# Kernel optimization log

Hardware: AMD Instinct MI355X
Metric: run time of the kernel (lower is better)

Reference implementation:

```python
import jax, jax.numpy as jnp
import numpy as np

NUM_HEADS = 4
NUM_GROUPS = 8
EPS = 1e-5


def setup_inputs() -> dict:
    key = jax.random.key(0)
    ks = jax.random.split(key, 5)
    B, C, H, W = 16, 512, 32, 32
    s = 1.0 / np.sqrt(C)
    return {
        "x": jax.random.normal(ks[0], (B, C, H, W), dtype=jnp.float32),
        "norm_w": jnp.ones((C,), jnp.float32),
        "norm_b": jnp.zeros((C,), jnp.float32),
        "q_w": jax.random.normal(ks[1], (C, C), jnp.float32) * s,
        "q_b": jnp.zeros((C,), jnp.float32),
        "k_w": jax.random.normal(ks[2], (C, C), jnp.float32) * s,
        "k_b": jnp.zeros((C,), jnp.float32),
        "v_w": jax.random.normal(ks[3], (C, C), jnp.float32) * s,
        "v_b": jnp.zeros((C,), jnp.float32),
        "p_w": jax.random.normal(ks[4], (C, C), jnp.float32) * s,
        "p_b": jnp.zeros((C,), jnp.float32),
    }


def _group_norm(x, w, b):
    # x: (B, C, N) -> GroupNorm over (C//G, N) per group
    B, C, N = x.shape
    g = x.reshape(B, NUM_GROUPS, C // NUM_GROUPS, N)
    mean = g.mean(axis=(2, 3), keepdims=True)
    var = g.var(axis=(2, 3), keepdims=True)
    g = (g - mean) * jax.lax.rsqrt(var + EPS)
    x = g.reshape(B, C, N)
    return x * w[None, :, None] + b[None, :, None]


def reference(x, norm_w, norm_b, q_w, q_b, k_w, k_b, v_w, v_b, p_w, p_b):
    B, C, H, W = x.shape
    N = H * W
    Ch = C // NUM_HEADS  # channels per head
    h = _group_norm(x.reshape(B, C, N), norm_w, norm_b)
    # 1x1 Conv1d == channel matmul: (o c, b c n -> b o n)
    q = jnp.einsum('oc,bcn->bon', q_w, h) + q_b[None, :, None]
    k = jnp.einsum('oc,bcn->bon', k_w, h) + k_b[None, :, None]
    v = jnp.einsum('oc,bcn->bon', v_w, h) + v_b[None, :, None]
    q = q.reshape(B, NUM_HEADS, Ch, N)
    k = k.reshape(B, NUM_HEADS, Ch, N)
    v = v.reshape(B, NUM_HEADS, Ch, N)
    attn = jnp.einsum('bhcn,bhcm->bhnm', q, k) * (1.0 / np.sqrt(Ch))
    attn = jax.nn.softmax(attn, axis=-1)
    out = jnp.einsum('bhnm,bhcm->bhcn', attn, v).reshape(B, C, N)
    out = jnp.einsum('oc,bcn->bon', p_w, out) + p_b[None, :, None]
    return x + out.reshape(B, C, H, W)
```

## Files before the change

kernel.cpp:

```cpp
#include <hip/hip_runtime.h>
#include <hip/hip_bf16.h>
#include <math.h>

#define B_    16
#define C_    512
#define N_    1024
#define G_    8
#define HEADS 4
#define CH    128
#define EPS   1e-5f

typedef __attribute__((ext_vector_type(8))) short short8;
typedef __attribute__((ext_vector_type(4))) float f32x4;
typedef __attribute__((ext_vector_type(16))) float f32x16;
typedef __attribute__((ext_vector_type(4))) int i32x4;

__device__ __forceinline__ unsigned short f2bf(float f) {
  union { float f; unsigned int i; } x; x.f = f;
  unsigned int r = x.i + 0x7FFFu + ((x.i >> 16) & 1u);
  return (unsigned short)(r >> 16);
}

__global__ __launch_bounds__(256) void gn_stats(const float* __restrict__ x,
                                                float* __restrict__ stats) {
  int bg = blockIdx.x;
  const float4* p4 = (const float4*)(x + (size_t)bg * (C_ / G_) * N_);
  const int n4 = (C_ / G_) * N_ / 4;
  float s = 0.f, ss = 0.f;
  for (int i = threadIdx.x; i < n4; i += 256) {
    float4 v = p4[i];
    s  += v.x + v.y + v.z + v.w;
    ss += v.x * v.x + v.y * v.y + v.z * v.z + v.w * v.w;
  }
  for (int o = 32; o; o >>= 1) { s += __shfl_down(s, o); ss += __shfl_down(ss, o); }
  __shared__ float ls[4], lss[4];
  int wid = threadIdx.x >> 6, lane = threadIdx.x & 63;
  if (lane == 0) { ls[wid] = s; lss[wid] = ss; }
  __syncthreads();
  if (threadIdx.x == 0) {
    float S = ls[0] + ls[1] + ls[2] + ls[3];
    float SS = lss[0] + lss[1] + lss[2] + lss[3];
    const float inv = 1.f / ((C_ / G_) * N_);
    float mean = S * inv;
    float var = SS * inv - mean * mean;
    stats[bg * 2]     = mean;
    stats[bg * 2 + 1] = rsqrtf(var + EPS);
  }
}

__global__ __launch_bounds__(256) void conv_w(const float* __restrict__ q, const float* __restrict__ k,
                                              const float* __restrict__ v, const float* __restrict__ p,
                                              const float* __restrict__ qb, const float* __restrict__ kb,
                                              unsigned short* __restrict__ dst,
                                              float* __restrict__ qkb) {
  const int n = C_ * C_;
  int i = blockIdx.x * 256 + threadIdx.x;
  if (i < n) {
    dst[i]         = f2bf(q[i]);
    dst[n + i]     = f2bf(k[i]);
    dst[2 * n + i] = f2bf(v[i]);
    dst[3 * n + i] = f2bf(p[i]);
  }
  if (i < 1024) qkb[i] = (i < 512) ? qb[i] : kb[i - 512];
}

__global__ __launch_bounds__(256) void gn_apply(const float* __restrict__ x,
                                                const float* __restrict__ stats,
                                                const float* __restrict__ gw,
                                                const float* __restrict__ gb,
                                                unsigned short* __restrict__ hT) {
  __shared__ float T[64][65];
  int b = blockIdx.z, c0 = blockIdx.y * 64, n0 = blockIdx.x * 64;
  int g = c0 / (C_ / G_);
  float mean = stats[(b * G_ + g) * 2], rstd = stats[(b * G_ + g) * 2 + 1];
  int t = threadIdx.x;
  for (int it = 0; it < 4; it++) {
    int L = it * 256 + t;
    int cc = L >> 4, nf = L & 15;
    float4 v = *(const float4*)&x[((size_t)b * C_ + c0 + cc) * N_ + n0 + nf * 4];
    float sw = gw[c0 + cc] * rstd, sb = gb[c0 + cc] - mean * sw;
    T[cc][nf * 4 + 0] = v.x * sw + sb;
    T[cc][nf * 4 + 1] = v.y * sw + sb;
    T[cc][nf * 4 + 2] = v.z * sw + sb;
    T[cc][nf * 4 + 3] = v.w * sw + sb;
  }
  __syncthreads();
  for (int it = 0; it < 4; it++) {
    int L = it * 256 + t;
    int nn = L >> 4, cv = L & 15;
    ushort4 o;
    o.x = f2bf(T[cv * 4 + 0][nn]);
    o.y = f2bf(T[cv * 4 + 1][nn]);
    o.z = f2bf(T[cv * 4 + 2][nn]);
    o.w = f2bf(T[cv * 4 + 3][nn]);
    *(ushort4*)&hT[((size_t)b * N_ + n0 + nn) * C_ + c0 + cv * 4] = o;
  }
}

template <bool OUT_BF16, bool BIAS_I, bool RESID>
__global__ __launch_bounds__(256) void gemm_tn(const unsigned short* __restrict__ A,
                                               const unsigned short* __restrict__ Bt,
                                               const float* __restrict__ bias,
                                               const float* __restrict__ resid,
                                               void* __restrict__ out,
                                               int Ncols, int K,
                                               long aBS, long bBS, long oBS) {
  __shared__ __align__(16) unsigned short As[128 * 64];
  __shared__ __align__(16) unsigned short Bs[128 * 64];
  const int b = blockIdx.z;
  const int i0 = blockIdx.y * 128, j0 = blockIdx.x * 128;
  const unsigned short* Ab = A + (size_t)b * aBS + (size_t)i0 * K;
  const unsigned short* Bb = Bt + (size_t)b * bBS + (size_t)j0 * K;
  const int t = threadIdx.x, w = t >> 6, l = t & 63;
  const int wi = (w >> 1) * 64, wj = (w & 1) * 64;
  const int lr = l & 15, lk = (l >> 4) * 8;
  const int srow = l >> 3, scol = (l & 7) * 8;

  f32x4 acc[4][4];
  const f32x4 zf = {0.f, 0.f, 0.f, 0.f};
#pragma unroll
  for (int m = 0; m < 4; m++)
#pragma unroll
    for (int n = 0; n < 4; n++) acc[m][n] = zf;

  for (int kt = 0; kt < K; kt += 64) {
    __syncthreads();
#pragma unroll
    for (int i = 0; i < 4; i++) {
      int seg = w * 4 + i;
      int row = seg * 8 + srow;
      __builtin_amdgcn_global_load_lds(
          (const __attribute__((address_space(1))) void*)&Ab[(size_t)row * K + kt + scol],
          (__attribute__((address_space(3))) void*)&As[seg * 512], 16, 0, 0);
      __builtin_amdgcn_global_load_lds(
          (const __attribute__((address_space(1))) void*)&Bb[(size_t)row * K + kt + scol],
          (__attribute__((address_space(3))) void*)&Bs[seg * 512], 16, 0, 0);
    }
    __syncthreads();
#pragma unroll
    for (int ks = 0; ks < 64; ks += 32) {
      short8 af[4], bf[4];
#pragma unroll
      for (int m = 0; m < 4; m++) af[m] = *(const short8*)&As[(wi + m * 16 + lr) * 64 + ks + lk];
#pragma unroll
      for (int n = 0; n < 4; n++) bf[n] = *(const short8*)&Bs[(wj + n * 16 + lr) * 64 + ks + lk];
#pragma unroll
      for (int m = 0; m < 4; m++)
#pragma unroll
        for (int n = 0; n < 4; n++)
          acc[m][n] = __builtin_amdgcn_mfma_f32_16x16x32_bf16(af[m], bf[n], acc[m][n], 0, 0, 0);
    }
  }

  int rbase = (l >> 4) * 4;
#pragma unroll
  for (int m = 0; m < 4; m++) {
    int ig = i0 + wi + m * 16 + rbase;
#pragma unroll
    for (int n = 0; n < 4; n++) {
      int jg = j0 + wj + n * 16 + lr;
#pragma unroll
      for (int r = 0; r < 4; r++) {
        float vv = acc[m][n][r];
        vv += BIAS_I ? bias[ig + r] : bias[jg];
        size_t oidx = (size_t)b * oBS + (size_t)(ig + r) * Ncols + jg;
        if (RESID) vv += resid[oidx];
        if (OUT_BF16) ((unsigned short*)out)[oidx] = f2bf(vv);
        else ((float*)out)[oidx] = vv;
      }
    }
  }
}

__global__ __launch_bounds__(256, 2) void attn_kernel(const unsigned short* __restrict__ qkT,
                                                      const unsigned short* __restrict__ v,
                                                      unsigned short* __restrict__ aoT) {
  __shared__ __align__(16) unsigned short Ks[2][64 * 128];
  __shared__ __align__(16) unsigned short Vs[2][128 * 64];
  const int t = threadIdx.x, w = t >> 6, l = t & 63;
  const int h = l >> 5, l31 = l & 31, l7 = l & 7;
  const int bh = blockIdx.y, b = bh >> 2, hd = bh & 3, c0h = hd * CH;
  const int qg = blockIdx.x * 128 + w * 32 + l31;
  const float sc2 = 0.08838834764831845f * 1.4426950408889634f;
  const float THRRAW = 11.5f / sc2;

  short8 qf[8];
  const unsigned short* qrow = qkT + ((size_t)b * N_ + qg) * 1024 + c0h;
#pragma unroll
  for (int kc = 0; kc < 8; kc++)
    qf[kc] = *(const short8*)&qrow[kc * 16 + h * 8];

  f32x16 o[4];
#pragma unroll
  for (int ct = 0; ct < 4; ct++) o[ct] = (f32x16)(0.f);
  float m = -INFINITY, lsum = 0.f;

  auto stage = [&](int cur, int tt) {
    int mt = tt * 64;
#pragma unroll
    for (int i = 0; i < 4; i++) {
      int seg = w * 4 + i;
      {
        int row = seg * 4 + (l >> 4);
        int gc = (l & 15) ^ (row & 7);
        const unsigned short* src = qkT + ((size_t)b * N_ + mt + row) * 1024 + 512 + c0h + gc * 8;
        __builtin_amdgcn_global_load_lds((const __attribute__((address_space(1))) void*)src,
                                         (__attribute__((address_space(3))) void*)&Ks[cur][seg * 512],
                                         16, 0, 0);
      }
      {
        int row = seg * 8 + (l >> 3);
        int gc = (l & 7) ^ (row & 7);
        const unsigned short* src = v + ((size_t)b * C_ + c0h + row) * N_ + mt + gc * 8;
        __builtin_amdgcn_global_load_lds((const __attribute__((address_space(1))) void*)src,
                                         (__attribute__((address_space(3))) void*)&Vs[cur][seg * 512],
                                         16, 0, 0);
      }
    }
  };

  stage(0, 0);

  for (int tt = 0; tt < 16; tt++) {
    int cur = tt & 1;
    __syncthreads();
    if (tt < 15) stage(cur ^ 1, tt + 1);

    f32x16 st0 = (f32x16)(0.f), st1 = (f32x16)(0.f);
    const unsigned short* KsB = &Ks[cur][0];
    __builtin_amdgcn_s_setprio(1);
#pragma unroll
    for (int kc = 0; kc < 8; kc++) {
      short8 kf0 = *(const short8*)&KsB[l31 * 128 + (((2 * kc + h) ^ l7) * 8)];
      short8 kf1 = *(const short8*)&KsB[(32 + l31) * 128 + (((2 * kc + h) ^ l7) * 8)];
      st0 = __builtin_amdgcn_mfma_f32_32x32x16_bf16(kf0, qf[kc], st0, 0, 0, 0);
      st1 = __builtin_amdgcn_mfma_f32_32x32x16_bf16(kf1, qf[kc], st1, 0, 0, 0);
    }
    __builtin_amdgcn_s_setprio(0);

    float tr[16];
#pragma unroll
    for (int r = 0; r < 16; r++) tr[r] = fmaxf(st0[r], st1[r]);
#pragma unroll
    for (int s = 8; s >= 1; s >>= 1)
#pragma unroll
      for (int r = 0; r < s; r++) tr[r] = fmaxf(tr[r], tr[r + s]);
    float pmax = fmaxf(tr[0], __shfl_xor(tr[0], 32));

    bool defer = (pmax <= m + THRRAW);
    bool skip = __all(defer);
    float mnew = skip ? m : fmaxf(m, pmax);
    float alpha = skip ? 1.f : exp2f((m - mnew) * sc2);
    float mb = mnew * sc2;
    m = mnew;

    float psg[4];
    short8 pf[4];
#pragma unroll
    for (int g = 0; g < 4; g++) {
      const int e0 = (g & 1) * 8;
      float p0, p1, p2, p3, p4, p5, p6, p7;
      if (g < 2) {
        p0 = exp2f(fmaf(st0[e0 + 0], sc2, -mb)); p1 = exp2f(fmaf(st0[e0 + 1], sc2, -mb));
        p2 = exp2f(fmaf(st0[e0 + 2], sc2, -mb)); p3 = exp2f(fmaf(st0[e0 + 3], sc2, -mb));
        p4 = exp2f(fmaf(st0[e0 + 4], sc2, -mb)); p5 = exp2f(fmaf(st0[e0 + 5], sc2, -mb));
        p6 = exp2f(fmaf(st0[e0 + 6], sc2, -mb)); p7 = exp2f(fmaf(st0[e0 + 7], sc2, -mb));
      } else {
        p0 = exp2f(fmaf(st1[e0 + 0], sc2, -mb)); p1 = exp2f(fmaf(st1[e0 + 1], sc2, -mb));
        p2 = exp2f(fmaf(st1[e0 + 2], sc2, -mb)); p3 = exp2f(fmaf(st1[e0 + 3], sc2, -mb));
        p4 = exp2f(fmaf(st1[e0 + 4], sc2, -mb)); p5 = exp2f(fmaf(st1[e0 + 5], sc2, -mb));
        p6 = exp2f(fmaf(st1[e0 + 6], sc2, -mb)); p7 = exp2f(fmaf(st1[e0 + 7], sc2, -mb));
      }
      float s01 = p0 + p1, s23 = p2 + p3, s45 = p4 + p5, s67 = p6 + p7;
      psg[g] = (s01 + s23) + (s45 + s67);
      unsigned int x, x2, y, y2;
      asm("v_cvt_pk_bf16_f32 %0, %1, %2" : "=v"(x)  : "v"(p0), "v"(p1));
      asm("v_cvt_pk_bf16_f32 %0, %1, %2" : "=v"(x2) : "v"(p2), "v"(p3));
      asm("v_cvt_pk_bf16_f32 %0, %1, %2" : "=v"(y)  : "v"(p4), "v"(p5));
      asm("v_cvt_pk_bf16_f32 %0, %1, %2" : "=v"(y2) : "v"(p6), "v"(p7));
      asm("v_permlane32_swap_b32 %0, %1" : "+v"(x), "+v"(y));
      asm("v_permlane32_swap_b32 %0, %1" : "+v"(x2), "+v"(y2));
      i32x4 pwv = {(int)x, (int)x2, (int)y, (int)y2};
      pf[g] = __builtin_bit_cast(short8, pwv);
    }
    float ps = (psg[0] + psg[1]) + (psg[2] + psg[3]);
    ps += __shfl_xor(ps, 32);
    lsum = lsum * alpha + ps;

    if (!skip) {
#pragma unroll
      for (int ct = 0; ct < 4; ct++)
#pragma unroll
        for (int r = 0; r < 16; r++) o[ct][r] *= alpha;
    }

    const unsigned short* VsB = &Vs[cur][0];
    __builtin_amdgcn_s_setprio(1);
#pragma unroll
    for (int ct = 0; ct < 4; ct++) {
#pragma unroll
      for (int g = 0; g < 4; g++) {
        short8 vf = *(const short8*)&VsB[(ct * 32 + l31) * 64 + (((2 * g + h) ^ l7) * 8)];
        o[ct] = __builtin_amdgcn_mfma_f32_32x32x16_bf16(vf, pf[g], o[ct], 0, 0, 0);
      }
    }
    __builtin_amdgcn_s_setprio(0);
  }

  float rn = 1.f / lsum;
  unsigned short* orow = aoT + ((size_t)b * N_ + qg) * C_ + c0h;
#pragma unroll
  for (int ct = 0; ct < 4; ct++)
#pragma unroll
    for (int u = 0; u < 4; u++) {
      ushort4 ov;
      ov.x = f2bf(o[ct][u * 4 + 0] * rn);
      ov.y = f2bf(o[ct][u * 4 + 1] * rn);
      ov.z = f2bf(o[ct][u * 4 + 2] * rn);
      ov.w = f2bf(o[ct][u * 4 + 3] * rn);
      *(ushort4*)&orow[ct * 32 + u * 8 + h * 4] = ov;
    }
}

extern "C" void kernel_launch(void* const* d_in, const int* in_sizes, int n_in,
                              void* d_out, int out_size, void* d_ws, size_t ws_size,
                              hipStream_t stream) {
  const float* x  = (const float*)d_in[0];
  const float* nw = (const float*)d_in[1];
  const float* nb = (const float*)d_in[2];
  const float* qw = (const float*)d_in[3];
  const float* qb = (const float*)d_in[4];
  const float* kw = (const float*)d_in[5];
  const float* kb = (const float*)d_in[6];
  const float* vw = (const float*)d_in[7];
  const float* vb = (const float*)d_in[8];
  const float* pw = (const float*)d_in[9];
  const float* pb = (const float*)d_in[10];

  char* ws = (char*)d_ws;
  unsigned short* wbf  = (unsigned short*)ws;
  float*          stats = (float*)(ws + 0x200000);
  float*          qkb  = (float*)(ws + 0x200800);
  unsigned short* hT   = (unsigned short*)(ws + 0x201000);
  unsigned short* qkT  = (unsigned short*)(ws + 0x1201000);
  unsigned short* vv   = (unsigned short*)(ws + 0x3201000);
  unsigned short* aoT  = hT;

  const long NC = (long)N_ * C_;
  const int n_w = C_ * C_;

  gn_stats<<<B_ * G_, 256, 0, stream>>>(x, stats);
  conv_w<<<n_w / 256, 256, 0, stream>>>(qw, kw, vw, pw, qb, kb, wbf, qkb);
  gn_apply<<<dim3(N_ / 64, C_ / 64, B_), 256, 0, stream>>>(x, stats, nw, nb, hT);

  gemm_tn<true, false, false><<<dim3(1024 / 128, N_ / 128, B_), 256, 0, stream>>>(
      hT, wbf, qkb, nullptr, qkT, 1024, C_, NC, 0, (long)N_ * 1024);
  gemm_tn<true, true, false><<<dim3(N_ / 128, C_ / 128, B_), 256, 0, stream>>>(
      wbf + 2 * n_w, hT, vb, nullptr, vv, N_, C_, 0, NC, NC);

  attn_kernel<<<dim3(N_ / 128, B_ * HEADS), 256, 0, stream>>>(qkT, vv, aoT);

  gemm_tn<false, true, true><<<dim3(N_ / 128, C_ / 128, B_), 256, 0, stream>>>(
      wbf + 3 * n_w, aoT, pb, x, d_out, N_, C_, 0, NC, NC);
}
```

Baseline: 165.8 us.

## Halve attention KV tile, raise occupancy, and remap grids for XCD locality

The attention kernel now processes 32 keys per iteration instead of 64, which halves its LDS footprint. Launch bounds go from 2 to 4 blocks per CU, and it uses new XOR swizzles with precomputed source pointers. The GEMM and attention launches switch to 1D grids with a block-index remap so that blocks sharing a batch or head land on the same XCD, aiming for better L2 reuse. The trade-off is twice as many loop iterations and barriers per block, and more register pressure at the higher occupancy target.

```diff
diff --git a/kernel.cpp b/kernel.cpp
--- a/kernel.cpp
+++ b/kernel.cpp
@@ -107,8 +107,11 @@
                                                long aBS, long bBS, long oBS) {
   __shared__ __align__(16) unsigned short As[128 * 64];
   __shared__ __align__(16) unsigned short Bs[128 * 64];
-  const int b = blockIdx.z;
-  const int i0 = blockIdx.y * 128, j0 = blockIdx.x * 128;
+  const int lin = blockIdx.x;
+  const int b = (lin & 7) * 2 + ((lin >> 3) & 1);
+  const int rest = lin >> 4;
+  const int bx = rest & 7, by = rest >> 3;
+  const int i0 = by * 128, j0 = bx * 128;
   const unsigned short* Ab = A + (size_t)b * aBS + (size_t)i0 * K;
   const unsigned short* Bb = Bt + (size_t)b * bBS + (size_t)j0 * K;
   const int t = threadIdx.x, w = t >> 6, l = t & 63;
@@ -172,107 +175,106 @@
   }
 }
 
-__global__ __launch_bounds__(256, 2) void attn_kernel(const unsigned short* __restrict__ qkT,
+__global__ __launch_bounds__(256, 4) void attn_kernel(const unsigned short* __restrict__ qkT,
                                                       const unsigned short* __restrict__ v,
                                                       unsigned short* __restrict__ aoT) {
-  __shared__ __align__(16) unsigned short Ks[2][64 * 128];
-  __shared__ __align__(16) unsigned short Vs[2][128 * 64];
+  __shared__ __align__(16) unsigned short Ks[2][32 * 128];
+  __shared__ __align__(16) unsigned short Vs[2][128 * 32];
   const int t = threadIdx.x, w = t >> 6, l = t & 63;
-  const int h = l >> 5, l31 = l & 31, l7 = l & 7;
-  const int bh = blockIdx.y, b = bh >> 2, hd = bh & 3, c0h = hd * CH;
-  const int qg = blockIdx.x * 128 + w * 32 + l31;
+  const int h = l >> 5, l31 = l & 31;
+  const int lin = blockIdx.x;
+  const int bh = (lin & 7) * 8 + ((lin >> 3) & 7);
+  const int qt = lin >> 6;
+  const int b = bh >> 2, hd = bh & 3, c0h = hd * CH;
+  const int qg = qt * 128 + w * 32 + l31;
   const float sc2 = 0.08838834764831845f * 1.4426950408889634f;
   const float THRRAW = 11.5f / sc2;
 
   short8 qf[8];
   const unsigned short* qrow = qkT + ((size_t)b * N_ + qg) * 1024 + c0h;
 #pragma unroll
-  for (int kc = 0; kc < 8; kc++)
-    qf[kc] = *(const short8*)&qrow[kc * 16 + h * 8];
+  for (int kc = 0; kc < 8; kc++) qf[kc] = *(const short8*)&qrow[kc * 16 + h * 8];
 
   f32x16 o[4];
 #pragma unroll
   for (int ct = 0; ct < 4; ct++) o[ct] = (f32x16)(0.f);
   float m = -INFINITY, lsum = 0.f;
 
-  auto stage = [&](int cur, int tt) {
-    int mt = tt * 64;
-#pragma unroll
-    for (int i = 0; i < 4; i++) {
-      int seg = w * 4 + i;
-      {
-        int row = seg * 4 + (l >> 4);
-        int gc = (l & 15) ^ (row & 7);
-        const unsigned short* src = qkT + ((size_t)b * N_ + mt + row) * 1024 + 512 + c0h + gc * 8;
-        __builtin_amdgcn_global_load_lds((const __attribute__((address_space(1))) void*)src,
-                                         (__attribute__((address_space(3))) void*)&Ks[cur][seg * 512],
-                                         16, 0, 0);
-      }
-      {
-        int row = seg * 8 + (l >> 3);
-        int gc = (l & 7) ^ (row & 7);
-        const unsigned short* src = v + ((size_t)b * C_ + c0h + row) * N_ + mt + gc * 8;
-        __builtin_amdgcn_global_load_lds((const __attribute__((address_space(1))) void*)src,
-                                         (__attribute__((address_space(3))) void*)&Vs[cur][seg * 512],
-                                         16, 0, 0);
-      }
+  const unsigned short* ksrc[2];
+  const unsigned short* vsrc[2];
+#pragma unroll
+  for (int i = 0; i < 2; i++) {
+    int seg = w * 2 + i;
+    int rowK = seg * 4 + (l >> 4);
+    int gcK = (l & 15) ^ (rowK & 15);
+    ksrc[i] = qkT + ((size_t)b * N_ + rowK) * 1024 + 512 + c0h + gcK * 8;
+    int rowV = seg * 16 + (l >> 2);
+    int gcV = (l & 3) ^ ((rowV >> 1) & 3);
+    vsrc[i] = v + ((size_t)b * C_ + c0h + rowV) * N_ + gcV * 8;
+  }
+
+  auto stage = [&](int cur) {
+    unsigned short* KsD = &Ks[cur][0];
+    unsigned short* VsD = &Vs[cur][0];
+#pragma unroll
+    for (int i = 0; i < 2; i++) {
+      int seg = w * 2 + i;
+      __builtin_amdgcn_global_load_lds((const __attribute__((address_space(1))) void*)ksrc[i],
+                                       (__attribute__((address_space(3))) void*)&KsD[seg * 512],
+                                       16, 0, 0);
+      ksrc[i] += 32 * 1024;
+      __builtin_amdgcn_global_load_lds((const __attribute__((address_space(1))) void*)vsrc[i],
+                                       (__attribute__((address_space(3))) void*)&VsD[seg * 512],
+                                       16, 0, 0);
+      vsrc[i] += 32;
     }
   };
 
-  stage(0, 0);
-
-  for (int tt = 0; tt < 16; tt++) {
+  stage(0);
+
+  const int kbase = l31 * 128 + (h ^ (l31 & 15)) * 8;
+  const int vbase = l31 * 32 + (h ^ ((l31 >> 1) & 3)) * 8;
+
+  for (int tt = 0; tt < 32; tt++) {
     int cur = tt & 1;
     __syncthreads();
-    if (tt < 15) stage(cur ^ 1, tt + 1);
-
-    f32x16 st0 = (f32x16)(0.f), st1 = (f32x16)(0.f);
+    if (tt < 31) stage(cur ^ 1);
+
+    f32x16 st = (f32x16)(0.f);
     const unsigned short* KsB = &Ks[cur][0];
     __builtin_amdgcn_s_setprio(1);
 #pragma unroll
     for (int kc = 0; kc < 8; kc++) {
-      short8 kf0 = *(const short8*)&KsB[l31 * 128 + (((2 * kc + h) ^ l7) * 8)];
-      short8 kf1 = *(const short8*)&KsB[(32 + l31) * 128 + (((2 * kc + h) ^ l7) * 8)];
-      st0 = __builtin_amdgcn_mfma_f32_32x32x16_bf16(kf0, qf[kc], st0, 0, 0, 0);
-      st1 = __builtin_amdgcn_mfma_f32_32x32x16_bf16(kf1, qf[kc], st1, 0, 0, 0);
+      short8 kf = *(const short8*)&KsB[kbase ^ (kc * 16)];
+      st = __builtin_amdgcn_mfma_f32_32x32x16_bf16(kf, qf[kc], st, 0, 0, 0);
     }
     __builtin_amdgcn_s_setprio(0);
 
-    float tr[16];
-#pragma unroll
-    for (int r = 0; r < 16; r++) tr[r] = fmaxf(st0[r], st1[r]);
-#pragma unroll
-    for (int s = 8; s >= 1; s >>= 1)
+    float tr[8];
+#pragma unroll
+    for (int r = 0; r < 8; r++) tr[r] = fmaxf(st[r], st[r + 8]);
+#pragma unroll
+    for (int s = 4; s >= 1; s >>= 1)
 #pragma unroll
       for (int r = 0; r < s; r++) tr[r] = fmaxf(tr[r], tr[r + s]);
     float pmax = fmaxf(tr[0], __shfl_xor(tr[0], 32));
 
-    bool defer = (pmax <= m + THRRAW);
-    bool skip = __all(defer);
+    bool skip = __all(pmax <= m + THRRAW);
     float mnew = skip ? m : fmaxf(m, pmax);
     float alpha = skip ? 1.f : exp2f((m - mnew) * sc2);
     float mb = mnew * sc2;
     m = mnew;
 
-    float psg[4];
-    short8 pf[4];
-#pragma unroll
-    for (int g = 0; g < 4; g++) {
-      const int e0 = (g & 1) * 8;
-      float p0, p1, p2, p3, p4, p5, p6, p7;
-      if (g < 2) {
-        p0 = exp2f(fmaf(st0[e0 + 0], sc2, -mb)); p1 = exp2f(fmaf(st0[e0 + 1], sc2, -mb));
-        p2 = exp2f(fmaf(st0[e0 + 2], sc2, -mb)); p3 = exp2f(fmaf(st0[e0 + 3], sc2, -mb));
-        p4 = exp2f(fmaf(st0[e0 + 4], sc2, -mb)); p5 = exp2f(fmaf(st0[e0 + 5], sc2, -mb));
-        p6 = exp2f(fmaf(st0[e0 + 6], sc2, -mb)); p7 = exp2f(fmaf(st0[e0 + 7], sc2, -mb));
-      } else {
-        p0 = exp2f(fmaf(st1[e0 + 0], sc2, -mb)); p1 = exp2f(fmaf(st1[e0 + 1], sc2, -mb));
-        p2 = exp2f(fmaf(st1[e0 + 2], sc2, -mb)); p3 = exp2f(fmaf(st1[e0 + 3], sc2, -mb));
-        p4 = exp2f(fmaf(st1[e0 + 4], sc2, -mb)); p5 = exp2f(fmaf(st1[e0 + 5], sc2, -mb));
-        p6 = exp2f(fmaf(st1[e0 + 6], sc2, -mb)); p7 = exp2f(fmaf(st1[e0 + 7], sc2, -mb));
-      }
-      float s01 = p0 + p1, s23 = p2 + p3, s45 = p4 + p5, s67 = p6 + p7;
-      psg[g] = (s01 + s23) + (s45 + s67);
+    float psg[2];
+    short8 pf[2];
+#pragma unroll
+    for (int g = 0; g < 2; g++) {
+      const int e0 = g * 8;
+      float p0 = exp2f(fmaf(st[e0 + 0], sc2, -mb)), p1 = exp2f(fmaf(st[e0 + 1], sc2, -mb));
+      float p2 = exp2f(fmaf(st[e0 + 2], sc2, -mb)), p3 = exp2f(fmaf(st[e0 + 3], sc2, -mb));
+      float p4 = exp2f(fmaf(st[e0 + 4], sc2, -mb)), p5 = exp2f(fmaf(st[e0 + 5], sc2, -mb));
+      float p6 = exp2f(fmaf(st[e0 + 6], sc2, -mb)), p7 = exp2f(fmaf(st[e0 + 7], sc2, -mb));
+      psg[g] = ((p0 + p1) + (p2 + p3)) + ((p4 + p5) + (p6 + p7));
       unsigned int x, x2, y, y2;
       asm("v_cvt_pk_bf16_f32 %0, %1, %2" : "=v"(x)  : "v"(p0), "v"(p1));
       asm("v_cvt_pk_bf16_f32 %0, %1, %2" : "=v"(x2) : "v"(p2), "v"(p3));
@@ -283,7 +285,7 @@
       i32x4 pwv = {(int)x, (int)x2, (int)y, (int)y2};
       pf[g] = __builtin_bit_cast(short8, pwv);
     }
-    float ps = (psg[0] + psg[1]) + (psg[2] + psg[3]);
+    float ps = psg[0] + psg[1];
     ps += __shfl_xor(ps, 32);
     lsum = lsum * alpha + ps;
 
@@ -299,8 +301,8 @@
 #pragma unroll
     for (int ct = 0; ct < 4; ct++) {
 #pragma unroll
-      for (int g = 0; g < 4; g++) {
-        short8 vf = *(const short8*)&VsB[(ct * 32 + l31) * 64 + (((2 * g + h) ^ l7) * 8)];
+      for (int g = 0; g < 2; g++) {
+        short8 vf = *(const short8*)&VsB[ct * 1024 + (vbase ^ (g * 16))];
         o[ct] = __builtin_amdgcn_mfma_f32_32x32x16_bf16(vf, pf[g], o[ct], 0, 0, 0);
       }
     }
@@ -353,13 +355,13 @@
   conv_w<<<n_w / 256, 256, 0, stream>>>(qw, kw, vw, pw, qb, kb, wbf, qkb);
   gn_apply<<<dim3(N_ / 64, C_ / 64, B_), 256, 0, stream>>>(x, stats, nw, nb, hT);
 
-  gemm_tn<true, false, false><<<dim3(1024 / 128, N_ / 128, B_), 256, 0, stream>>>(
+  gemm_tn<true, false, false><<<dim3(1024), 256, 0, stream>>>(
       hT, wbf, qkb, nullptr, qkT, 1024, C_, NC, 0, (long)N_ * 1024);
-  gemm_tn<true, true, false><<<dim3(N_ / 128, C_ / 128, B_), 256, 0, stream>>>(
+  gemm_tn<true, true, false><<<dim3(512), 256, 0, stream>>>(
       wbf + 2 * n_w, hT, vb, nullptr, vv, N_, C_, 0, NC, NC);
 
-  attn_kernel<<<dim3(N_ / 128, B_ * HEADS), 256, 0, stream>>>(qkT, vv, aoT);
-
-  gemm_tn<false, true, true><<<dim3(N_ / 128, C_ / 128, B_), 256, 0, stream>>>(
+  attn_kernel<<<dim3(512), 256, 0, stream>>>(qkT, vv, aoT);
+
+  gemm_tn<false, true, true><<<dim3(512), 256, 0, stream>>>(
       wbf + 3 * n_w, aoT, pb, x, d_out, N_, C_, 0, NC, NC);
 }
```

Measured after the change: 197.7 us. 19.2% more time.
